# Performance work log

Hardware: AMD Instinct MI355X
Metric: run time of the kernel (lower is better)

Reference implementation:

```python
import jax, jax.numpy as jnp
import numpy as np

EPS = 1e-7
B, N, DIM, NH, HD, WIN, HASH_WIN = 2, 1024, 512, 8, 64, 64, 8


def expmap0(v, c):
    sqrt_c = jnp.clip(jnp.sqrt(c), EPS)
    v_norm = jnp.linalg.norm(v, axis=-1, keepdims=True)
    is_zero = v_norm < EPS
    safe = jnp.clip(v_norm, EPS)
    mag = jnp.tanh(sqrt_c * safe) / sqrt_c
    return jnp.where(is_zero, jnp.zeros_like(v), mag * (v / safe))


def poincare_dist(x, y, c):
    # x: (B,H,N,1,D), y: (B,H,N,W,D), c: (B,1,1,1,1) -> (B,H,N,W)
    sqrt_c = jnp.clip(jnp.sqrt(c), EPS)
    x2 = jnp.sum(x * x, -1, keepdims=True)
    y2 = jnp.sum(y * y, -1, keepdims=True)
    xy = jnp.sum(x * y, -1, keepdims=True)
    num = (1 - 2 * c * xy + c * y2) * x + (1 - c * x2) * (-y)
    den = 1 - 2 * c * xy + c * c * x2 * y2
    diff = num / jnp.clip(den, EPS)
    dn = jnp.linalg.norm(diff, axis=-1)
    arg = jnp.minimum(jnp.squeeze(sqrt_c, -1) * jnp.clip(dn, EPS), 1.0 - EPS)
    return 2.0 * jnp.arctanh(arg) / jnp.squeeze(sqrt_c, -1)


def sliding_windows(t, w):
    # t: (B,H,N,D) -> (B,H,N,w,D), left-padded causal window
    Bb, H, Nn, D = t.shape
    pad = jnp.zeros((Bb, H, w - 1, D), t.dtype)
    tp = jnp.concatenate([pad, t], axis=2)
    idx = jnp.arange(w)[None, :] + jnp.arange(Nn)[:, None]  # (N,w)
    return tp[:, :, idx, :]


def layernorm(x, s, b):
    m = jnp.mean(x, -1, keepdims=True)
    v = jnp.var(x, -1, keepdims=True)
    return (x - m) / jnp.sqrt(v + 1e-6) * s + b


def rope(x, cos, sin):
    # x: (B,N,H,hd), cos/sin: (N, hd//2) -- complex rotation in real arithmetic
    xr, xi = jnp.split(x, 2, axis=-1)
    cos = cos[None, :, None, :]
    sin = sin[None, :, None, :]
    return jnp.concatenate([xr * cos - xi * sin, xr * sin + xi * cos], axis=-1)


def setup_inputs() -> dict:
    key = jax.random.key(0)
    ks = jax.random.split(key, 10)
    x = jax.random.normal(ks[0], (B, N, DIM), jnp.float32)
    pos = jnp.arange(N, dtype=jnp.float32)
    inv = 1.0 / (10000.0 ** (jnp.arange(0, HD, 2, dtype=jnp.float32) / HD))
    ang = pos[:, None] * inv[None, :]  # (N, HD//2)
    freqs_cos, freqs_sin = jnp.cos(ang), jnp.sin(ang)
    c = jax.random.uniform(ks[1], (B,), jnp.float32) * 0.9 + 0.1
    s = 0.02
    Wq = jax.random.normal(ks[2], (DIM, DIM), jnp.float32) * s
    Wk = jax.random.normal(ks[3], (DIM, DIM), jnp.float32) * s
    Wv = jax.random.normal(ks[4], (DIM, DIM), jnp.float32) * s
    Wo = jax.random.normal(ks[5], (DIM, DIM), jnp.float32) * s
    W1 = jax.random.normal(ks[6], (DIM, 4 * DIM), jnp.float32) * s
    W2 = jax.random.normal(ks[7], (4 * DIM, DIM), jnp.float32) * s
    bq = jnp.zeros((DIM,)); bk = jnp.zeros((DIM,)); bv = jnp.zeros((DIM,))
    bo = jnp.zeros((DIM,)); b1 = jnp.zeros((4 * DIM,)); b2 = jnp.zeros((DIM,))
    ln1_s = jnp.ones((DIM,)); ln1_b = jnp.zeros((DIM,))
    ln2_s = jnp.ones((DIM,)); ln2_b = jnp.zeros((DIM,))
    geo_scale = jnp.ones((NH, 1, 1), jnp.float32)
    hash_offset = jax.random.normal(ks[8], (1, 1, NH, HD), jnp.float32) * 0.01
    return dict(x=x, freqs_cos=freqs_cos, freqs_sin=freqs_sin, c=c,
                Wq=Wq, bq=bq, Wk=Wk, bk=bk, Wv=Wv, bv=bv, Wo=Wo, bo=bo,
                W1=W1, b1=b1, W2=W2, b2=b2,
                ln1_s=ln1_s, ln1_b=ln1_b, ln2_s=ln2_s, ln2_b=ln2_b,
                geo_scale=geo_scale, hash_offset=hash_offset)


def reference(x, freqs_cos, freqs_sin, c, Wq, bq, Wk, bk, Wv, bv, Wo, bo,
              W1, b1, W2, b2, ln1_s, ln1_b, ln2_s, ln2_b, geo_scale, hash_offset):
    x_res = x
    xn = layernorm(x, ln1_s, ln1_b)
    q = (xn @ Wq + bq).reshape(B, N, NH, HD)
    k = (xn @ Wk + bk).reshape(B, N, NH, HD)
    v = (xn @ Wv + bv).reshape(B, N, NH, HD)
    q = q + hash_offset * jnp.log(1.0 + HASH_WIN)
    q_rot = rope(q, freqs_cos, freqs_sin)
    k_rot = rope(k, freqs_cos, freqs_sin)
    c_b = c.reshape(B, 1, 1, 1)
    q_h = expmap0(q_rot, c_b)
    k_h = expmap0(k_rot, c_b)
    q_h, k_h, v = (t.transpose(0, 2, 1, 3) for t in (q_h, k_h, v))  # (B,H,N,D)
    k_win = sliding_windows(k_h, WIN)  # (B,H,N,W,D)
    v_win = sliding_windows(v, WIN)
    dist = poincare_dist(q_h[:, :, :, None, :], k_win, c.reshape(B, 1, 1, 1, 1))  # (B,H,N,W)
    scores = -geo_scale * dist
    w = jax.nn.softmax(scores, axis=-1)
    attn = jnp.einsum('bhnw,bhnwd->bhnd', w, v_win)
    attn = attn.transpose(0, 2, 1, 3).reshape(B, N, DIM)
    x_out = x_res + (attn @ Wo + bo)
    h = layernorm(x_out, ln2_s, ln2_b)
    ffn = jax.nn.gelu(h @ W1 + b1) @ W2 + b2
    return x_out + ffn
```

## Files before the change

kernel.cpp:

```cpp
#include <hip/hip_runtime.h>
#include <math.h>
#include <stdint.h>

#define Bn   2
#define Nn   1024
#define DIMn 512
#define NHn  8
#define HDn  64
#define QKVS 1536
#define EPSF 1e-7f

typedef __attribute__((ext_vector_type(8))) short short8;
typedef __attribute__((ext_vector_type(4))) float floatx4;

__device__ __forceinline__ unsigned short f2bf(float f) {
  union { float f; uint32_t u; } v; v.f = f;
  uint32_t u = v.u;
  return (unsigned short)((u + 0x7FFFu + ((u >> 16) & 1u)) >> 16);
}
__device__ __forceinline__ float bf2f(unsigned short h) {
  union { uint32_t u; float f; } v; v.u = ((uint32_t)h) << 16;
  return v.f;
}

__device__ __forceinline__ float wsum(float v) {
#pragma unroll
  for (int m = 32; m >= 1; m >>= 1) v += __shfl_xor(v, m, 64);
  return v;
}
__device__ __forceinline__ float wmax(float v) {
#pragma unroll
  for (int m = 32; m >= 1; m >>= 1) v = fmaxf(v, __shfl_xor(v, m, 64));
  return v;
}

__device__ __forceinline__ float gelu_tanh(float x) {
  const float k0 = 0.7978845608028654f;
  float x3 = x * x * x;
  return 0.5f * x * (1.f + tanhf(k0 * (x + 0.044715f * x3)));
}

__device__ __forceinline__ void glds16(const unsigned short* g, unsigned short* l) {
  __builtin_amdgcn_global_load_lds((const __attribute__((address_space(1))) void*)g,
                                   (__attribute__((address_space(3))) void*)l, 16, 0, 0);
}

__global__ __launch_bounds__(256) void prep_kernel(
    const float* __restrict__ Wq, const float* __restrict__ Wk,
    const float* __restrict__ Wv, const float* __restrict__ Wo,
    const float* __restrict__ W1, const float* __restrict__ W2,
    unsigned short* __restrict__ Wcat_hi, unsigned short* __restrict__ Wcat_lo,
    unsigned short* __restrict__ Wo_t, unsigned short* __restrict__ W1_t,
    unsigned short* __restrict__ W2_t,
    const float* __restrict__ bq, const float* __restrict__ bk,
    const float* __restrict__ bv, float* __restrict__ bias_cat,
    const float* __restrict__ x, const float* __restrict__ ln1s,
    const float* __restrict__ ln1b,
    unsigned short* __restrict__ xn_hi, unsigned short* __restrict__ xn_lo) {
  __shared__ float t[32][33];
  __shared__ float red[2][4];
  int bid = blockIdx.x;
  int tid = threadIdx.x;
  if (bid == 3072) {
    for (int i = tid; i < 512; i += 256) {
      bias_cat[i] = bq[i];
      bias_cat[512 + i] = bk[i];
      bias_cat[1024 + i] = bv[i];
    }
    return;
  }
  if (bid > 3072) {
    int row = bid - 3073;
    const float* xr = x + (size_t)row * DIMn;
    float2 xv = *(const float2*)(xr + tid * 2);
    float s  = xv.x + xv.y;
    float s2 = xv.x * xv.x + xv.y * xv.y;
    s = wsum(s); s2 = wsum(s2);
    int wv = tid >> 6;
    if ((tid & 63) == 0) { red[0][wv] = s; red[1][wv] = s2; }
    __syncthreads();
    s  = red[0][0] + red[0][1] + red[0][2] + red[0][3];
    s2 = red[1][0] + red[1][1] + red[1][2] + red[1][3];
    float mean = s * (1.f / DIMn);
    float var  = s2 * (1.f / DIMn) - mean * mean;
    float rstd = rsqrtf(var + 1e-6f);
    int d = tid * 2;
    float2 gv = *(const float2*)(ln1s + d);
    float2 bv2 = *(const float2*)(ln1b + d);
    float o0 = (xv.x - mean) * rstd * gv.x + bv2.x;
    float o1 = (xv.y - mean) * rstd * gv.y + bv2.y;
    size_t idx = (size_t)row * DIMn + d;
    unsigned short h0 = f2bf(o0), h1 = f2bf(o1);
    ushort2 hv; hv.x = h0; hv.y = h1;
    *(ushort2*)(xn_hi + idx) = hv;
    ushort2 lv; lv.x = f2bf(o0 - bf2f(h0)); lv.y = f2bf(o1 - bf2f(h1));
    *(ushort2*)(xn_lo + idx) = lv;
    return;
  }
  const float* W;
  unsigned short* hi;
  unsigned short* lo = nullptr;
  int K, N, tix;
  if (bid < 256)       { W = Wq; hi = Wcat_hi;               lo = Wcat_lo;               K = 512;  N = 512;  tix = bid; }
  else if (bid < 512)  { W = Wk; hi = Wcat_hi + 512 * 512;   lo = Wcat_lo + 512 * 512;   K = 512;  N = 512;  tix = bid - 256; }
  else if (bid < 768)  { W = Wv; hi = Wcat_hi + 1024 * 512;  K = 512;  N = 512;  tix = bid - 512; }
  else if (bid < 1024) { W = Wo; hi = Wo_t;                  K = 512;  N = 512;  tix = bid - 768; }
  else if (bid < 2048) { W = W1; hi = W1_t;                  K = 512;  N = 2048; tix = bid - 1024; }
  else                 { W = W2; hi = W2_t;                  K = 2048; N = 512;  tix = bid - 2048; }
  int ntn = N >> 5;
  int kt = tix / ntn, nt = tix - kt * ntn;
  int k0 = kt * 32, n0 = nt * 32;
  for (int i = tid; i < 1024; i += 256) {
    int r = i >> 5, c = i & 31;
    t[r][c] = W[(size_t)(k0 + r) * N + n0 + c];
  }
  __syncthreads();
  for (int i = tid; i < 1024; i += 256) {
    int r = i >> 5, c = i & 31;
    float v = t[c][r];
    unsigned short h = f2bf(v);
    size_t oi = (size_t)(n0 + r) * K + k0 + c;
    hi[oi] = h;
    if (lo) lo[oi] = f2bf(v - bf2f(h));
  }
}

__global__ __launch_bounds__(256) void ln_kernel(const float* __restrict__ x,
                                                 const float* __restrict__ g,
                                                 const float* __restrict__ be,
                                                 unsigned short* __restrict__ yhi) {
  __shared__ float red[2][4];
  int row = blockIdx.x;
  int tid = threadIdx.x;
  const float* xr = x + (size_t)row * DIMn;
  float2 xv = *(const float2*)(xr + tid * 2);
  float s  = xv.x + xv.y;
  float s2 = xv.x * xv.x + xv.y * xv.y;
  s = wsum(s); s2 = wsum(s2);
  int wv = tid >> 6;
  if ((tid & 63) == 0) { red[0][wv] = s; red[1][wv] = s2; }
  __syncthreads();
  s  = red[0][0] + red[0][1] + red[0][2] + red[0][3];
  s2 = red[1][0] + red[1][1] + red[1][2] + red[1][3];
  float mean = s * (1.f / DIMn);
  float var  = s2 * (1.f / DIMn) - mean * mean;
  float rstd = rsqrtf(var + 1e-6f);
  int d = tid * 2;
  float2 gv = *(const float2*)(g + d);
  float2 bv = *(const float2*)(be + d);
  float o0 = (xv.x - mean) * rstd * gv.x + bv.x;
  float o1 = (xv.y - mean) * rstd * gv.y + bv.y;
  size_t idx = (size_t)row * DIMn + d;
  ushort2 hv; hv.x = f2bf(o0); hv.y = f2bf(o1);
  *(ushort2*)(yhi + idx) = hv;
}

template <int BM, int BN, int BKT, int SPLIT, int EPI, int OUTBF16>
__global__ __launch_bounds__(256) void gemm_mfma(
    const unsigned short* __restrict__ Ahi, const unsigned short* __restrict__ Alo,
    const unsigned short* __restrict__ Bhi, const unsigned short* __restrict__ Blo,
    const float* __restrict__ bias, const float* __restrict__ res,
    void* __restrict__ outp, int M, int N, int K) {
  constexpr int FI = BM / 32, FJ = BN / 32;
  constexpr int AE = BM * BKT, BE = BN * BKT;
  constexpr int NB = (SPLIT > 0) ? 2 : 1;
  constexpr int CPR = BKT / 8;
  constexpr int ACH = BM * CPR, BCH = BN * CPR;
  __shared__ unsigned short smem[NB * (AE + BE)];
  unsigned short* AsHi = smem;
  unsigned short* AsLo = smem + ((SPLIT > 0) ? AE : 0);
  unsigned short* BsHi = smem + NB * AE;
  unsigned short* BsLo = BsHi + ((SPLIT > 0) ? BE : 0);

  int tid = threadIdx.x;
  int lane = tid & 63;
  int wid = tid >> 6;
  int wm = (wid >> 1) * (BM / 2), wn = (wid & 1) * (BN / 2);
  int bm = blockIdx.y * BM, bn = blockIdx.x * BN;
  int m16 = lane & 15, kg = lane >> 4;
  bool dos = (SPLIT == 1) || (SPLIT == 2 && bn < 1024);

  floatx4 acc[FI][FJ];
#pragma unroll
  for (int i = 0; i < FI; ++i)
#pragma unroll
    for (int j = 0; j < FJ; ++j) { floatx4 z = {0.f, 0.f, 0.f, 0.f}; acc[i][j] = z; }

  const unsigned short* aph = Ahi + (size_t)bm * K;
  const unsigned short* bph = Bhi + (size_t)bn * K;
  const unsigned short* apl = (SPLIT > 0) ? (Alo + (size_t)bm * K) : nullptr;
  const unsigned short* bpl = (SPLIT > 0) ? (Blo + (size_t)bn * K) : nullptr;

  for (int k0 = 0; k0 < K; k0 += BKT) {
#pragma unroll
    for (int c = tid; c < ACH; c += 256) {
      int row = c / CPR, kk = (c % CPR) * 8;
      glds16(aph + (size_t)row * K + k0 + kk, AsHi + c * 8);
      if (SPLIT > 0 && dos) glds16(apl + (size_t)row * K + k0 + kk, AsLo + c * 8);
    }
#pragma unroll
    for (int c = tid; c < BCH; c += 256) {
      int row = c / CPR, kk = (c % CPR) * 8;
      glds16(bph + (size_t)row * K + k0 + kk, BsHi + c * 8);
      if (SPLIT > 0 && dos) glds16(bpl + (size_t)row * K + k0 + kk, BsLo + c * 8);
    }
    __syncthreads();

#pragma unroll
    for (int ks = 0; ks < BKT / 32; ++ks) {
      short8 ah[FI], bh[FJ];
      short8 al[(SPLIT > 0) ? FI : 1], bl[(SPLIT > 0) ? FJ : 1];
#pragma unroll
      for (int i = 0; i < FI; ++i) {
        int r = wm + i * 16 + m16;
        ah[i] = *(const short8*)&AsHi[r * BKT + ks * 32 + kg * 8];
        if (SPLIT > 0 && dos) al[i] = *(const short8*)&AsLo[r * BKT + ks * 32 + kg * 8];
      }
#pragma unroll
      for (int j = 0; j < FJ; ++j) {
        int r = wn + j * 16 + m16;
        bh[j] = *(const short8*)&BsHi[r * BKT + ks * 32 + kg * 8];
        if (SPLIT > 0 && dos) bl[j] = *(const short8*)&BsLo[r * BKT + ks * 32 + kg * 8];
      }
#pragma unroll
      for (int i = 0; i < FI; ++i)
#pragma unroll
        for (int j = 0; j < FJ; ++j) {
          acc[i][j] = __builtin_amdgcn_mfma_f32_16x16x32_bf16(ah[i], bh[j], acc[i][j], 0, 0, 0);
          if (SPLIT > 0) {
            if (dos) {
              acc[i][j] = __builtin_amdgcn_mfma_f32_16x16x32_bf16(al[i], bh[j], acc[i][j], 0, 0, 0);
              acc[i][j] = __builtin_amdgcn_mfma_f32_16x16x32_bf16(ah[i], bl[j], acc[i][j], 0, 0, 0);
            }
          }
        }
    }
    __syncthreads();
  }

#pragma unroll
  for (int i = 0; i < FI; ++i) {
    int gr0 = bm + wm + i * 16 + kg * 4;
#pragma unroll
    for (int j = 0; j < FJ; ++j) {
      int gc = bn + wn + j * 16 + m16;
      float bsv = bias[gc];
#pragma unroll
      for (int r = 0; r < 4; ++r) {
        size_t idx = (size_t)(gr0 + r) * N + gc;
        float v = acc[i][j][r] + bsv;
        if constexpr (EPI == 1) v += res[idx];
        if constexpr (EPI == 2) v = gelu_tanh(v);
        if constexpr (OUTBF16) ((unsigned short*)outp)[idx] = f2bf(v);
        else ((float*)outp)[idx] = v;
      }
    }
  }
}

__global__ __launch_bounds__(512) void attn_fused(const float* __restrict__ qkv,
                                                  const float* __restrict__ fcos,
                                                  const float* __restrict__ fsin,
                                                  const float* __restrict__ cvec,
                                                  const float* __restrict__ geo,
                                                  const float* __restrict__ hash,
                                                  unsigned short* __restrict__ attn_out) {
  __shared__ unsigned short Qhi[32][72], Qlo[32][72];
  __shared__ unsigned short Khi[96][72], Klo[96][72];
  __shared__ unsigned short Vt[64][104];
  __shared__ unsigned short Pb[32][104];
  __shared__ float Sf[32][97];
  __shared__ float x2s[32], bxs[32], y2s[96], gys[96];

  int tid = threadIdx.x, lane = tid & 63, wv = tid >> 6;
  int bid = blockIdx.x;
  int nt = bid & 31, h = (bid >> 5) & 7, b = bid >> 8;
  int n0 = nt * 32;
  float c = cvec[b];
  float sqc = sqrtf(c);
  float rsqc = 1.f / sqc;
  float gs = geo[h];
  int dr = lane & 31;
  bool hih = lane >= 32;
  const float LOG9 = 2.1972245773362196f;
  float hofr = hash[h * HDn + dr] * LOG9;
  float hofi = hash[h * HDn + dr + 32] * LOG9;

  for (int i = tid; i < 32 * 52; i += 512) ((uint32_t*)Pb)[i] = 0u;

#pragma unroll
  for (int i = 0; i < 4; ++i) {
    int q = wv * 4 + i;
    int n = n0 + q;
    size_t bas = (size_t)(b * Nn + n) * QKVS + h * HDn;
    float qr = qkv[bas + dr] + hofr;
    float qi = qkv[bas + dr + 32] + hofi;
    float cs = fcos[n * 32 + dr], sn = fsin[n * 32 + dr];
    float qv = hih ? (qr * sn + qi * cs) : (qr * cs - qi * sn);
    float nq = sqrtf(wsum(qv * qv));
    float sq = fmaxf(nq, EPSF);
    float t = sqc * sq;
    float em = expf(-2.f * t);
    float opem = 1.f + em;
    float mag = ((1.f - em) / opem) * rsqc;
    float sech2 = 4.f * em / (opem * opem);
    float oq = (nq < EPSF) ? 0.f : mag * (qv / sq);
    unsigned short hh = f2bf(oq);
    Qhi[q][lane] = hh;
    Qlo[q][lane] = f2bf(oq - bf2f(hh));
    if (lane == 0) {
      x2s[q] = (nq < EPSF) ? 0.f : mag * mag;
      bxs[q] = (nq < EPSF) ? 1.f : sech2;
    }
  }
#pragma unroll 4
  for (int i = 0; i < 12; ++i) {
    int r = wv * 12 + i;
    int gi = n0 - 64 + r;
    float ok = 0.f, vf = 0.f, y2 = 0.f, gy = 1.f;
    if (gi >= 0) {
      size_t bas = (size_t)(b * Nn + gi) * QKVS + h * HDn;
      float kr = qkv[bas + 512 + dr];
      float ki = qkv[bas + 512 + dr + 32];
      vf = qkv[bas + 1024 + lane];
      float cs = fcos[gi * 32 + dr], sn = fsin[gi * 32 + dr];
      float kv = hih ? (kr * sn + ki * cs) : (kr * cs - ki * sn);
      float nk = sqrtf(wsum(kv * kv));
      float sk = fmaxf(nk, EPSF);
      float t = sqc * sk;
      float em = expf(-2.f * t);
      float opem = 1.f + em;
      float mag = ((1.f - em) / opem) * rsqc;
      float sech2 = 4.f * em / (opem * opem);
      ok = (nk < EPSF) ? 0.f : mag * (kv / sk);
      y2 = (nk < EPSF) ? 0.f : mag * mag;
      gy = (nk < EPSF) ? 1.f : sech2;
    }
    unsigned short hh = f2bf(ok);
    Khi[r][lane] = hh;
    Klo[r][lane] = f2bf(ok - bf2f(hh));
    Vt[lane][r] = f2bf(vf);
    if (lane == 0) { y2s[r] = y2; gys[r] = gy; }
  }
  __syncthreads();

  int m16 = lane & 15, kg = lane >> 4;
#pragma unroll
  for (int uu = 0; uu < 2; ++uu) {
    int u = wv + uu * 8;
    if (u < 12) {
      int mt = u / 6, ntile = u % 6;
      floatx4 acc = {0.f, 0.f, 0.f, 0.f};
#pragma unroll
      for (int ks = 0; ks < 2; ++ks) {
        short8 ah = *(const short8*)&Qhi[mt * 16 + m16][ks * 32 + kg * 8];
        short8 al = *(const short8*)&Qlo[mt * 16 + m16][ks * 32 + kg * 8];
        short8 bh = *(const short8*)&Khi[ntile * 16 + m16][ks * 32 + kg * 8];
        short8 bl = *(const short8*)&Klo[ntile * 16 + m16][ks * 32 + kg * 8];
        acc = __builtin_amdgcn_mfma_f32_16x16x32_bf16(ah, bh, acc, 0, 0, 0);
        acc = __builtin_amdgcn_mfma_f32_16x16x32_bf16(al, bh, acc, 0, 0, 0);
        acc = __builtin_amdgcn_mfma_f32_16x16x32_bf16(ah, bl, acc, 0, 0, 0);
      }
#pragma unroll
      for (int r = 0; r < 4; ++r) Sf[mt * 16 + kg * 4 + r][ntile * 16 + m16] = acc[r];
    }
  }
  __syncthreads();

#pragma unroll
  for (int i = 0; i < 4; ++i) {
    int nl = wv * 4 + i;
    int r = nl + 1 + lane;
    float xy = Sf[nl][r];
    float x2 = x2s[nl], y2 = y2s[r];
    float bx = bxs[nl], gy = gys[r];

    float den = fmaf(c * c * x2, y2, fmaf(-2.f * c, xy, 1.f));
    den = fmaxf(den, EPSF);
    float rden = 1.f / den;
    float s2 = fmaxf(x2 - 2.f * xy + y2, 0.f);
    float z = sqrtf(c * s2 * rden);
    float omz2 = bx * gy * rden;
    float opz = 1.f + fminf(z, 1.f);
    float ratio = fminf(opz * opz / omz2, 1.9999999e7f);
    float sc = -gs * logf(ratio) * rsqc;

    float mx = wmax(sc);
    float e = expf(sc - mx);
    float se = wsum(e);
    Pb[nl][r] = f2bf(e / se);
  }
  __syncthreads();

  {
    int mt = wv >> 2, ntile = wv & 3;
    floatx4 acc = {0.f, 0.f, 0.f, 0.f};
#pragma unroll
    for (int ks = 0; ks < 3; ++ks) {
      short8 a = *(const short8*)&Pb[mt * 16 + m16][ks * 32 + kg * 8];
      short8 bb = *(const short8*)&Vt[ntile * 16 + m16][ks * 32 + kg * 8];
      acc = __builtin_amdgcn_mfma_f32_16x16x32_bf16(a, bb, acc, 0, 0, 0);
    }
#pragma unroll
    for (int r = 0; r < 4; ++r) {
      int qrow = mt * 16 + kg * 4 + r;
      int d = ntile * 16 + m16;
      attn_out[(size_t)(b * Nn + n0 + qrow) * DIMn + h * HDn + d] = f2bf(acc[r]);
    }
  }
}

extern "C" void kernel_launch(void* const* d_in, const int* in_sizes, int n_in,
                              void* d_out, int out_size, void* d_ws, size_t ws_size,
                              hipStream_t stream) {
  const float* x    = (const float*)d_in[0];
  const float* fcos = (const float*)d_in[1];
  const float* fsin = (const float*)d_in[2];
  const float* cvec = (const float*)d_in[3];
  const float* Wq = (const float*)d_in[4];  const float* bq = (const float*)d_in[5];
  const float* Wk = (const float*)d_in[6];  const float* bk = (const float*)d_in[7];
  const float* Wv = (const float*)d_in[8];  const float* bv = (const float*)d_in[9];
  const float* Wo = (const float*)d_in[10]; const float* bo = (const float*)d_in[11];
  const float* W1 = (const float*)d_in[12]; const float* b1 = (const float*)d_in[13];
  const float* W2 = (const float*)d_in[14]; const float* b2 = (const float*)d_in[15];
  const float* ln1s = (const float*)d_in[16]; const float* ln1b = (const float*)d_in[17];
  const float* ln2s = (const float*)d_in[18]; const float* ln2b = (const float*)d_in[19];
  const float* geo  = (const float*)d_in[20]; const float* hash = (const float*)d_in[21];
  float* out = (float*)d_out;
  char* base = (char*)d_ws;

  unsigned short* Wcat_hi = (unsigned short*)(base + 0);
  unsigned short* Wcat_lo = (unsigned short*)(base + 1572864);
  unsigned short* Wo_t    = (unsigned short*)(base + 3145728);
  unsigned short* W1_t    = (unsigned short*)(base + 3670016);
  unsigned short* W2_t    = (unsigned short*)(base + 5767168);
  unsigned short* xn_hi   = (unsigned short*)(base + 7864320);
  unsigned short* xn_lo   = (unsigned short*)(base + 9961472);
  float*          qkv     = (float*)(base + 12058624);
  unsigned short* attnb   = (unsigned short*)(base + 7864320);
  float*          xout    = (float*)(base + 9961472);
  unsigned short* hbuf    = (unsigned short*)(base + 14155776);
  unsigned short* mid     = (unsigned short*)(base + 16252928);
  float*          bias_cat= (float*)(base + 24641536);

  const int M = Bn * Nn;

  prep_kernel<<<3073 + M, 256, 0, stream>>>(Wq, Wk, Wv, Wo, W1, W2, Wcat_hi, Wcat_lo,
                                            Wo_t, W1_t, W2_t, bq, bk, bv, bias_cat,
                                            x, ln1s, ln1b, xn_hi, xn_lo);
  gemm_mfma<64, 64, 32, 2, 0, 0><<<dim3(QKVS / 64, M / 64), 256, 0, stream>>>(
      xn_hi, xn_lo, Wcat_hi, Wcat_lo, bias_cat, nullptr, qkv, M, QKVS, 512);
  attn_fused<<<Bn * NHn * (Nn / 32), 512, 0, stream>>>(qkv, fcos, fsin, cvec, geo, hash, attnb);
  gemm_mfma<32, 64, 64, 0, 1, 0><<<dim3(DIMn / 64, M / 32), 256, 0, stream>>>(
      attnb, nullptr, Wo_t, nullptr, bo, x, xout, M, DIMn, 512);
  ln_kernel<<<M, 256, 0, stream>>>(xout, ln2s, ln2b, hbuf);
  gemm_mfma<64, 128, 64, 0, 2, 1><<<dim3(2048 / 128, M / 64), 256, 0, stream>>>(
      hbuf, nullptr, W1_t, nullptr, b1, nullptr, mid, M, 2048, 512);
  gemm_mfma<32, 64, 64, 0, 1, 0><<<dim3(DIMn / 64, M / 32), 256, 0, stream>>>(
      mid, nullptr, W2_t, nullptr, b2, xout, out, M, DIMn, 2048);
}
```

Measured before the change: 194.2 us.

## Fuse LayerNorm2 into FFN1 GEMM prologue and deepen K tiles for output GEMMs

Removes the standalone ln_kernel and its bf16 hbuf round trip. A new ffn1_ln kernel computes per-row mean and rstd for its 64-row tile, then normalizes fp32 xout on the fly while filling shared memory before the MFMA loop. Each of the 16 column blocks now recomputes the row statistics and rereads fp32 activations instead of bf16, which trades extra global reads for one fewer launch and one fewer intermediate write. Separately, the Wo and W2 GEMMs use a K tile of 128 instead of 64.

Result: slower. 215.4 us (+11.0%).

```diff
diff --git a/kernel.cpp b/kernel.cpp
--- a/kernel.cpp
+++ b/kernel.cpp
@@ -125,36 +125,6 @@
   }
 }
 
-__global__ __launch_bounds__(256) void ln_kernel(const float* __restrict__ x,
-                                                 const float* __restrict__ g,
-                                                 const float* __restrict__ be,
-                                                 unsigned short* __restrict__ yhi) {
-  __shared__ float red[2][4];
-  int row = blockIdx.x;
-  int tid = threadIdx.x;
-  const float* xr = x + (size_t)row * DIMn;
-  float2 xv = *(const float2*)(xr + tid * 2);
-  float s  = xv.x + xv.y;
-  float s2 = xv.x * xv.x + xv.y * xv.y;
-  s = wsum(s); s2 = wsum(s2);
-  int wv = tid >> 6;
-  if ((tid & 63) == 0) { red[0][wv] = s; red[1][wv] = s2; }
-  __syncthreads();
-  s  = red[0][0] + red[0][1] + red[0][2] + red[0][3];
-  s2 = red[1][0] + red[1][1] + red[1][2] + red[1][3];
-  float mean = s * (1.f / DIMn);
-  float var  = s2 * (1.f / DIMn) - mean * mean;
-  float rstd = rsqrtf(var + 1e-6f);
-  int d = tid * 2;
-  float2 gv = *(const float2*)(g + d);
-  float2 bv = *(const float2*)(be + d);
-  float o0 = (xv.x - mean) * rstd * gv.x + bv.x;
-  float o1 = (xv.y - mean) * rstd * gv.y + bv.y;
-  size_t idx = (size_t)row * DIMn + d;
-  ushort2 hv; hv.x = f2bf(o0); hv.y = f2bf(o1);
-  *(ushort2*)(yhi + idx) = hv;
-}
-
 template <int BM, int BN, int BKT, int SPLIT, int EPI, int OUTBF16>
 __global__ __launch_bounds__(256) void gemm_mfma(
     const unsigned short* __restrict__ Ahi, const unsigned short* __restrict__ Alo,
@@ -253,6 +223,113 @@
         if constexpr (EPI == 2) v = gelu_tanh(v);
         if constexpr (OUTBF16) ((unsigned short*)outp)[idx] = f2bf(v);
         else ((float*)outp)[idx] = v;
+      }
+    }
+  }
+}
+
+__global__ __launch_bounds__(256) void ffn1_ln(
+    const float* __restrict__ xout, const float* __restrict__ g,
+    const float* __restrict__ be,
+    const unsigned short* __restrict__ W1t, const float* __restrict__ b1,
+    unsigned short* __restrict__ mid) {
+  constexpr int BM = 64, BN = 128, BK = 64;
+  constexpr int AST = BK + 8;
+  __shared__ unsigned short As[BM * AST];
+  __shared__ unsigned short Bs[BN * BK];
+  __shared__ float mrs[BM][2];
+
+  int tid = threadIdx.x, lane = tid & 63, wid = tid >> 6;
+  int bm = blockIdx.y * BM, bn = blockIdx.x * BN;
+  int m16 = lane & 15, kg = lane >> 4;
+  int wm = (wid >> 1) * (BM / 2), wn = (wid & 1) * (BN / 2);
+
+#pragma unroll 4
+  for (int i = 0; i < 16; ++i) {
+    int row = wid * 16 + i;
+    const float* xr = xout + (size_t)(bm + row) * DIMn;
+    float4 a = ((const float4*)xr)[lane * 2];
+    float4 b = ((const float4*)xr)[lane * 2 + 1];
+    float s  = a.x + a.y + a.z + a.w + b.x + b.y + b.z + b.w;
+    float s2 = a.x*a.x + a.y*a.y + a.z*a.z + a.w*a.w + b.x*b.x + b.y*b.y + b.z*b.z + b.w*b.w;
+    s = wsum(s); s2 = wsum(s2);
+    if (lane == 0) {
+      float mean = s * (1.f / DIMn);
+      float var  = s2 * (1.f / DIMn) - mean * mean;
+      mrs[row][0] = mean;
+      mrs[row][1] = rsqrtf(var + 1e-6f);
+    }
+  }
+  __syncthreads();
+
+  floatx4 acc[2][4];
+#pragma unroll
+  for (int i = 0; i < 2; ++i)
+#pragma unroll
+    for (int j = 0; j < 4; ++j) { floatx4 z = {0.f, 0.f, 0.f, 0.f}; acc[i][j] = z; }
+
+  for (int k0 = 0; k0 < DIMn; k0 += BK) {
+    {
+      int row = tid >> 2, c0 = (tid & 3) * 16;
+      const float* xr = xout + (size_t)(bm + row) * DIMn + k0 + c0;
+      float mean = mrs[row][0], rstd = mrs[row][1];
+      unsigned short* dst = &As[row * AST + c0];
+#pragma unroll
+      for (int j = 0; j < 2; ++j) {
+        float4 v0 = ((const float4*)xr)[j * 2];
+        float4 v1 = ((const float4*)xr)[j * 2 + 1];
+        float4 g0 = ((const float4*)(g + k0 + c0))[j * 2];
+        float4 g1 = ((const float4*)(g + k0 + c0))[j * 2 + 1];
+        float4 e0 = ((const float4*)(be + k0 + c0))[j * 2];
+        float4 e1 = ((const float4*)(be + k0 + c0))[j * 2 + 1];
+        short8 o;
+        o[0] = (short)f2bf((v0.x - mean) * rstd * g0.x + e0.x);
+        o[1] = (short)f2bf((v0.y - mean) * rstd * g0.y + e0.y);
+        o[2] = (short)f2bf((v0.z - mean) * rstd * g0.z + e0.z);
+        o[3] = (short)f2bf((v0.w - mean) * rstd * g0.w + e0.w);
+        o[4] = (short)f2bf((v1.x - mean) * rstd * g1.x + e1.x);
+        o[5] = (short)f2bf((v1.y - mean) * rstd * g1.y + e1.y);
+        o[6] = (short)f2bf((v1.z - mean) * rstd * g1.z + e1.z);
+        o[7] = (short)f2bf((v1.w - mean) * rstd * g1.w + e1.w);
+        *(short8*)(dst + j * 8) = o;
+      }
+    }
+#pragma unroll
+    for (int c = tid; c < BN * 8; c += 256) {
+      int row = c >> 3, kk = (c & 7) * 8;
+      glds16(W1t + (size_t)(bn + row) * DIMn + k0 + kk, Bs + c * 8);
+    }
+    __syncthreads();
+
+#pragma unroll
+    for (int ks = 0; ks < 2; ++ks) {
+      short8 ah[2], bh[4];
+#pragma unroll
+      for (int i = 0; i < 2; ++i)
+        ah[i] = *(const short8*)&As[(wm + i * 16 + m16) * AST + ks * 32 + kg * 8];
+#pragma unroll
+      for (int j = 0; j < 4; ++j)
+        bh[j] = *(const short8*)&Bs[(wn + j * 16 + m16) * BK + ks * 32 + kg * 8];
+#pragma unroll
+      for (int i = 0; i < 2; ++i)
+#pragma unroll
+        for (int j = 0; j < 4; ++j)
+          acc[i][j] = __builtin_amdgcn_mfma_f32_16x16x32_bf16(ah[i], bh[j], acc[i][j], 0, 0, 0);
+    }
+    __syncthreads();
+  }
+
+#pragma unroll
+  for (int i = 0; i < 2; ++i) {
+    int gr0 = bm + wm + i * 16 + kg * 4;
+#pragma unroll
+    for (int j = 0; j < 4; ++j) {
+      int gc = bn + wn + j * 16 + m16;
+      float bsv = b1[gc];
+#pragma unroll
+      for (int r = 0; r < 4; ++r) {
+        float v = gelu_tanh(acc[i][j][r] + bsv);
+        mid[(size_t)(gr0 + r) * 2048 + gc] = f2bf(v);
       }
     }
   }
@@ -439,7 +516,6 @@
   float*          qkv     = (float*)(base + 12058624);
   unsigned short* attnb   = (unsigned short*)(base + 7864320);
   float*          xout    = (float*)(base + 9961472);
-  unsigned short* hbuf    = (unsigned short*)(base + 14155776);
   unsigned short* mid     = (unsigned short*)(base + 16252928);
   float*          bias_cat= (float*)(base + 24641536);
 
@@ -451,11 +527,10 @@
   gemm_mfma<64, 64, 32, 2, 0, 0><<<dim3(QKVS / 64, M / 64), 256, 0, stream>>>(
       xn_hi, xn_lo, Wcat_hi, Wcat_lo, bias_cat, nullptr, qkv, M, QKVS, 512);
   attn_fused<<<Bn * NHn * (Nn / 32), 512, 0, stream>>>(qkv, fcos, fsin, cvec, geo, hash, attnb);
-  gemm_mfma<32, 64, 64, 0, 1, 0><<<dim3(DIMn / 64, M / 32), 256, 0, stream>>>(
+  gemm_mfma<32, 64, 128, 0, 1, 0><<<dim3(DIMn / 64, M / 32), 256, 0, stream>>>(
       attnb, nullptr, Wo_t, nullptr, bo, x, xout, M, DIMn, 512);
-  ln_kernel<<<M, 256, 0, stream>>>(xout, ln2s, ln2b, hbuf);
-  gemm_mfma<64, 128, 64, 0, 2, 1><<<dim3(2048 / 128, M / 64), 256, 0, stream>>>(
-      hbuf, nullptr, W1_t, nullptr, b1, nullptr, mid, M, 2048, 512);
-  gemm_mfma<32, 64, 64, 0, 1, 0><<<dim3(DIMn / 64, M / 32), 256, 0, stream>>>(
+  ffn1_ln<<<dim3(2048 / 128, M / 64), 256, 0, stream>>>(
+      xout, ln2s, ln2b, W1_t, b1, mid);
+  gemm_mfma<32, 64, 128, 0, 1, 0><<<dim3(DIMn / 64, M / 32), 256, 0, stream>>>(
       mid, nullptr, W2_t, nullptr, b2, xout, out, M, DIMn, 2048);
 }
```

## Fuse all stages into one persistent cooperative megakernel with grid syncs

Applied to the files above, without the earlier changes.

Replaces the seven separate kernel launches (prep, QKV GEMM, attention, out-proj, layernorm, FFN GEMMs) with a single cooperative kernel that loops over work units per stage and uses grid.sync between stages. The intent is to remove launch overhead and inter-kernel gaps for this small, latency-bound problem. It trades that for grid-wide barrier cost, 512-thread blocks reusing one shared-memory union, and a grid capped at 512 blocks, which can leave stages with fewer tiles than their previous launches. The old multi-kernel path is kept as a fallback if the cooperative launch fails.

New measurement: 477.4 us. +145.9%, slower.

```diff
diff --git a/kernel.cpp b/kernel.cpp
--- a/kernel.cpp
+++ b/kernel.cpp
@@ -1,4 +1,5 @@
 #include <hip/hip_runtime.h>
+#include <hip/hip_cooperative_groups.h>
 #include <math.h>
 #include <stdint.h>
 
@@ -13,6 +14,8 @@
 typedef __attribute__((ext_vector_type(8))) short short8;
 typedef __attribute__((ext_vector_type(4))) float floatx4;
 
+namespace cg = cooperative_groups;
+
 __device__ __forceinline__ unsigned short f2bf(float f) {
   union { float f; uint32_t u; } v; v.f = f;
   uint32_t u = v.u;
@@ -43,6 +46,378 @@
 __device__ __forceinline__ void glds16(const unsigned short* g, unsigned short* l) {
   __builtin_amdgcn_global_load_lds((const __attribute__((address_space(1))) void*)g,
                                    (__attribute__((address_space(3))) void*)l, 16, 0, 0);
+}
+
+struct MegaArgs {
+  const float *x, *fcos, *fsin, *cvec;
+  const float *Wq, *bq, *Wk, *bk, *Wv, *bv, *Wo, *bo, *W1, *b1, *W2, *b2;
+  const float *ln1s, *ln1b, *ln2s, *ln2b, *geo, *hash;
+  float* out;
+  unsigned short *Wcat_hi, *Wcat_lo, *Wo_t, *W1_t, *W2_t;
+  unsigned short *xn_hi, *xn_lo, *attnb, *hbuf, *mid;
+  float *qkv, *xout, *bias_cat;
+};
+
+struct AttnSm {
+  unsigned short Qhi[32][72], Qlo[32][72];
+  unsigned short Khi[96][72], Klo[96][72];
+  unsigned short Vt[64][104];
+  unsigned short Pb[32][104];
+  float Sf[32][97];
+  float x2s[32], bxs[32], y2s[96], gys[96];
+};
+struct PrepSm { float t[32][33]; float red[2][8]; };
+union MegaSm {
+  PrepSm prep;
+  AttnSm attn;
+  unsigned short gbuf[12288];
+};
+
+template <int BM, int BN, int BKT, int SPLIT, int EPI, int OUTBF16>
+__device__ void gemm_tile(unsigned short* sbuf, int bm, int bn,
+    const unsigned short* __restrict__ Ahi, const unsigned short* __restrict__ Alo,
+    const unsigned short* __restrict__ Bhi, const unsigned short* __restrict__ Blo,
+    const float* __restrict__ bias, const float* __restrict__ res,
+    void* __restrict__ outp, int N, int K, int tid) {
+  constexpr int FI = BM / 32, FJ = BN / 64;
+  constexpr int AE = BM * BKT, BE = BN * BKT;
+  constexpr int NB = (SPLIT > 0) ? 2 : 1;
+  constexpr int CPR = BKT / 8;
+  constexpr int ACH = BM * CPR, BCH = BN * CPR;
+  unsigned short* AsHi = sbuf;
+  unsigned short* AsLo = sbuf + ((SPLIT > 0) ? AE : 0);
+  unsigned short* BsHi = sbuf + NB * AE;
+  unsigned short* BsLo = BsHi + ((SPLIT > 0) ? BE : 0);
+
+  int lane = tid & 63, wid = tid >> 6;
+  int wm = (wid >> 2) * (BM / 2), wn = (wid & 3) * (BN / 4);
+  int m16 = lane & 15, kg = lane >> 4;
+  bool dos = (SPLIT == 1) || (SPLIT == 2 && bn < 1024);
+
+  floatx4 acc[FI][FJ];
+#pragma unroll
+  for (int i = 0; i < FI; ++i)
+#pragma unroll
+    for (int j = 0; j < FJ; ++j) { floatx4 z = {0.f, 0.f, 0.f, 0.f}; acc[i][j] = z; }
+
+  const unsigned short* aph = Ahi + (size_t)bm * K;
+  const unsigned short* bph = Bhi + (size_t)bn * K;
+  const unsigned short* apl = (SPLIT > 0) ? (Alo + (size_t)bm * K) : nullptr;
+  const unsigned short* bpl = (SPLIT > 0) ? (Blo + (size_t)bn * K) : nullptr;
+
+  for (int k0 = 0; k0 < K; k0 += BKT) {
+    for (int c = tid; c < ACH; c += 512) {
+      int row = c / CPR, kk = (c % CPR) * 8;
+      glds16(aph + (size_t)row * K + k0 + kk, AsHi + c * 8);
+      if (SPLIT > 0 && dos) glds16(apl + (size_t)row * K + k0 + kk, AsLo + c * 8);
+    }
+    for (int c = tid; c < BCH; c += 512) {
+      int row = c / CPR, kk = (c % CPR) * 8;
+      glds16(bph + (size_t)row * K + k0 + kk, BsHi + c * 8);
+      if (SPLIT > 0 && dos) glds16(bpl + (size_t)row * K + k0 + kk, BsLo + c * 8);
+    }
+    __syncthreads();
+
+#pragma unroll
+    for (int ks = 0; ks < BKT / 32; ++ks) {
+      short8 ah[FI], bh[FJ];
+      short8 al[(SPLIT > 0) ? FI : 1], bl[(SPLIT > 0) ? FJ : 1];
+#pragma unroll
+      for (int i = 0; i < FI; ++i) {
+        int r = wm + i * 16 + m16;
+        ah[i] = *(const short8*)&AsHi[r * BKT + ks * 32 + kg * 8];
+        if (SPLIT > 0 && dos) al[i] = *(const short8*)&AsLo[r * BKT + ks * 32 + kg * 8];
+      }
+#pragma unroll
+      for (int j = 0; j < FJ; ++j) {
+        int r = wn + j * 16 + m16;
+        bh[j] = *(const short8*)&BsHi[r * BKT + ks * 32 + kg * 8];
+        if (SPLIT > 0 && dos) bl[j] = *(const short8*)&BsLo[r * BKT + ks * 32 + kg * 8];
+      }
+#pragma unroll
+      for (int i = 0; i < FI; ++i)
+#pragma unroll
+        for (int j = 0; j < FJ; ++j) {
+          acc[i][j] = __builtin_amdgcn_mfma_f32_16x16x32_bf16(ah[i], bh[j], acc[i][j], 0, 0, 0);
+          if (SPLIT > 0 && dos) {
+            acc[i][j] = __builtin_amdgcn_mfma_f32_16x16x32_bf16(al[i], bh[j], acc[i][j], 0, 0, 0);
+            acc[i][j] = __builtin_amdgcn_mfma_f32_16x16x32_bf16(ah[i], bl[j], acc[i][j], 0, 0, 0);
+          }
+        }
+    }
+    __syncthreads();
+  }
+
+#pragma unroll
+  for (int i = 0; i < FI; ++i) {
+    int gr0 = bm + wm + i * 16 + kg * 4;
+#pragma unroll
+    for (int j = 0; j < FJ; ++j) {
+      int gc = bn + wn + j * 16 + m16;
+      float bsv = bias[gc];
+#pragma unroll
+      for (int r = 0; r < 4; ++r) {
+        size_t idx = (size_t)(gr0 + r) * N + gc;
+        float v = acc[i][j][r] + bsv;
+        if constexpr (EPI == 1) v += res[idx];
+        if constexpr (EPI == 2) v = gelu_tanh(v);
+        if constexpr (OUTBF16) ((unsigned short*)outp)[idx] = f2bf(v);
+        else ((float*)outp)[idx] = v;
+      }
+    }
+  }
+}
+
+__global__ __launch_bounds__(512, 4) void mega(MegaArgs A) {
+  cg::grid_group grid = cg::this_grid();
+  __shared__ MegaSm sm;
+  int tid = threadIdx.x;
+  int lane = tid & 63, wid = tid >> 6;
+  int nblk = gridDim.x;
+
+  for (int u = blockIdx.x; u < 3073 + 2048; u += nblk) {
+    if (u == 3072) {
+      if (tid < 512) {
+        A.bias_cat[tid] = A.bq[tid];
+        A.bias_cat[512 + tid] = A.bk[tid];
+        A.bias_cat[1024 + tid] = A.bv[tid];
+      }
+    } else if (u > 3072) {
+      int row = u - 3073;
+      const float* xr = A.x + (size_t)row * DIMn;
+      float xv = xr[tid];
+      float s = wsum(xv), s2 = wsum(xv * xv);
+      if (lane == 0) { sm.prep.red[0][wid] = s; sm.prep.red[1][wid] = s2; }
+      __syncthreads();
+      s = 0.f; s2 = 0.f;
+#pragma unroll
+      for (int w = 0; w < 8; ++w) { s += sm.prep.red[0][w]; s2 += sm.prep.red[1][w]; }
+      float mean = s * (1.f / DIMn);
+      float var  = s2 * (1.f / DIMn) - mean * mean;
+      float rstd = rsqrtf(var + 1e-6f);
+      float o = (xv - mean) * rstd * A.ln1s[tid] + A.ln1b[tid];
+      size_t idx = (size_t)row * DIMn + tid;
+      unsigned short h = f2bf(o);
+      A.xn_hi[idx] = h;
+      A.xn_lo[idx] = f2bf(o - bf2f(h));
+      __syncthreads();
+    } else {
+      const float* W;
+      unsigned short* hi;
+      unsigned short* lo = nullptr;
+      int K, N, tix;
+      if (u < 256)       { W = A.Wq; hi = A.Wcat_hi;              lo = A.Wcat_lo;              K = 512;  N = 512;  tix = u; }
+      else if (u < 512)  { W = A.Wk; hi = A.Wcat_hi + 512 * 512;  lo = A.Wcat_lo + 512 * 512;  K = 512;  N = 512;  tix = u - 256; }
+      else if (u < 768)  { W = A.Wv; hi = A.Wcat_hi + 1024 * 512; K = 512;  N = 512;  tix = u - 512; }
+      else if (u < 1024) { W = A.Wo; hi = A.Wo_t;                 K = 512;  N = 512;  tix = u - 768; }
+      else if (u < 2048) { W = A.W1; hi = A.W1_t;                 K = 512;  N = 2048; tix = u - 1024; }
+      else               { W = A.W2; hi = A.W2_t;                 K = 2048; N = 512;  tix = u - 2048; }
+      int ntn = N >> 5;
+      int kt = tix / ntn, nt = tix - kt * ntn;
+      int k0 = kt * 32, n0 = nt * 32;
+      for (int i = tid; i < 1024; i += 512) {
+        int r = i >> 5, c = i & 31;
+        sm.prep.t[r][c] = W[(size_t)(k0 + r) * N + n0 + c];
+      }
+      __syncthreads();
+      for (int i = tid; i < 1024; i += 512) {
+        int r = i >> 5, c = i & 31;
+        float v = sm.prep.t[c][r];
+        unsigned short h = f2bf(v);
+        size_t oi = (size_t)(n0 + r) * K + k0 + c;
+        hi[oi] = h;
+        if (lo) lo[oi] = f2bf(v - bf2f(h));
+      }
+      __syncthreads();
+    }
+  }
+  grid.sync();
+
+  for (int u = blockIdx.x; u < 768; u += nblk) {
+    int ty = u / 24, tx = u - ty * 24;
+    gemm_tile<64, 64, 32, 2, 0, 0>(sm.gbuf, ty * 64, tx * 64,
+        A.xn_hi, A.xn_lo, A.Wcat_hi, A.Wcat_lo, A.bias_cat, nullptr,
+        A.qkv, QKVS, 512, tid);
+  }
+  grid.sync();
+
+  for (int u = blockIdx.x; u < 512; u += nblk) {
+    AttnSm& at = sm.attn;
+    int nt = u & 31, h = (u >> 5) & 7, b = u >> 8;
+    int n0 = nt * 32;
+    float c = A.cvec[b];
+    float sqc = sqrtf(c);
+    float rsqc = 1.f / sqc;
+    float gs = A.geo[h];
+    int dr = lane & 31;
+    bool hih = lane >= 32;
+    const float LOG9 = 2.1972245773362196f;
+    float hofr = A.hash[h * HDn + dr] * LOG9;
+    float hofi = A.hash[h * HDn + dr + 32] * LOG9;
+
+    for (int i = tid; i < 32 * 52; i += 512) ((uint32_t*)at.Pb)[i] = 0u;
+
+#pragma unroll
+    for (int i = 0; i < 4; ++i) {
+      int q = wid * 4 + i;
+      int n = n0 + q;
+      size_t bas = (size_t)(b * Nn + n) * QKVS + h * HDn;
+      float qr = A.qkv[bas + dr] + hofr;
+      float qi = A.qkv[bas + dr + 32] + hofi;
+      float cs = A.fcos[n * 32 + dr], sn = A.fsin[n * 32 + dr];
+      float qv = hih ? (qr * sn + qi * cs) : (qr * cs - qi * sn);
+      float nq = sqrtf(wsum(qv * qv));
+      float sq = fmaxf(nq, EPSF);
+      float t = sqc * sq;
+      float em = expf(-2.f * t);
+      float opem = 1.f + em;
+      float mag = ((1.f - em) / opem) * rsqc;
+      float sech2 = 4.f * em / (opem * opem);
+      float oq = (nq < EPSF) ? 0.f : mag * (qv / sq);
+      unsigned short hh = f2bf(oq);
+      at.Qhi[q][lane] = hh;
+      at.Qlo[q][lane] = f2bf(oq - bf2f(hh));
+      if (lane == 0) {
+        at.x2s[q] = (nq < EPSF) ? 0.f : mag * mag;
+        at.bxs[q] = (nq < EPSF) ? 1.f : sech2;
+      }
+    }
+#pragma unroll 4
+    for (int i = 0; i < 12; ++i) {
+      int r = wid * 12 + i;
+      int gi = n0 - 64 + r;
+      float ok = 0.f, vf = 0.f, y2 = 0.f, gy = 1.f;
+      if (gi >= 0) {
+        size_t bas = (size_t)(b * Nn + gi) * QKVS + h * HDn;
+        float kr = A.qkv[bas + 512 + dr];
+        float ki = A.qkv[bas + 512 + dr + 32];
+        vf = A.qkv[bas + 1024 + lane];
+        float cs = A.fcos[gi * 32 + dr], sn = A.fsin[gi * 32 + dr];
+        float kv = hih ? (kr * sn + ki * cs) : (kr * cs - ki * sn);
+        float nk = sqrtf(wsum(kv * kv));
+        float sk = fmaxf(nk, EPSF);
+        float t = sqc * sk;
+        float em = expf(-2.f * t);
+        float opem = 1.f + em;
+        float mag = ((1.f - em) / opem) * rsqc;
+        float sech2 = 4.f * em / (opem * opem);
+        ok = (nk < EPSF) ? 0.f : mag * (kv / sk);
+        y2 = (nk < EPSF) ? 0.f : mag * mag;
+        gy = (nk < EPSF) ? 1.f : sech2;
+      }
+      unsigned short hh = f2bf(ok);
+      at.Khi[r][lane] = hh;
+      at.Klo[r][lane] = f2bf(ok - bf2f(hh));
+      at.Vt[lane][r] = f2bf(vf);
+      if (lane == 0) { at.y2s[r] = y2; at.gys[r] = gy; }
+    }
+    __syncthreads();
+
+    int m16 = lane & 15, kg = lane >> 4;
+#pragma unroll
+    for (int uu = 0; uu < 2; ++uu) {
+      int tu = wid + uu * 8;
+      if (tu < 12) {
+        int mt = tu / 6, ntile = tu % 6;
+        floatx4 acc = {0.f, 0.f, 0.f, 0.f};
+#pragma unroll
+        for (int ks = 0; ks < 2; ++ks) {
+          short8 ah = *(const short8*)&at.Qhi[mt * 16 + m16][ks * 32 + kg * 8];
+          short8 al = *(const short8*)&at.Qlo[mt * 16 + m16][ks * 32 + kg * 8];
+          short8 bh = *(const short8*)&at.Khi[ntile * 16 + m16][ks * 32 + kg * 8];
+          short8 bl = *(const short8*)&at.Klo[ntile * 16 + m16][ks * 32 + kg * 8];
+          acc = __builtin_amdgcn_mfma_f32_16x16x32_bf16(ah, bh, acc, 0, 0, 0);
+          acc = __builtin_amdgcn_mfma_f32_16x16x32_bf16(al, bh, acc, 0, 0, 0);
+          acc = __builtin_amdgcn_mfma_f32_16x16x32_bf16(ah, bl, acc, 0, 0, 0);
+        }
+#pragma unroll
+        for (int r = 0; r < 4; ++r) at.Sf[mt * 16 + kg * 4 + r][ntile * 16 + m16] = acc[r];
+      }
+    }
+    __syncthreads();
+
+#pragma unroll
+    for (int i = 0; i < 4; ++i) {
+      int nl = wid * 4 + i;
+      int r = nl + 1 + lane;
+      float xy = at.Sf[nl][r];
+      float x2 = at.x2s[nl], y2 = at.y2s[r];
+      float bx = at.bxs[nl], gy = at.gys[r];
+
+      float den = fmaf(c * c * x2, y2, fmaf(-2.f * c, xy, 1.f));
+      den = fmaxf(den, EPSF);
+      float rden = 1.f / den;
+      float s2 = fmaxf(x2 - 2.f * xy + y2, 0.f);
+      float z = sqrtf(c * s2 * rden);
+      float omz2 = bx * gy * rden;
+      float opz = 1.f + fminf(z, 1.f);
+      float ratio = fminf(opz * opz / omz2, 1.9999999e7f);
+      float sc = -gs * logf(ratio) * rsqc;
+
+      float mx = wmax(sc);
+      float e = expf(sc - mx);
+      float se = wsum(e);
+      at.Pb[nl][r] = f2bf(e / se);
+    }
+    __syncthreads();
+
+    {
+      int mt = wid >> 2, ntile = wid & 3;
+      floatx4 acc = {0.f, 0.f, 0.f, 0.f};
+#pragma unroll
+      for (int ks = 0; ks < 3; ++ks) {
+        short8 a = *(const short8*)&at.Pb[mt * 16 + m16][ks * 32 + kg * 8];
+        short8 bb = *(const short8*)&at.Vt[ntile * 16 + m16][ks * 32 + kg * 8];
+        acc = __builtin_amdgcn_mfma_f32_16x16x32_bf16(a, bb, acc, 0, 0, 0);
+      }
+#pragma unroll
+      for (int r = 0; r < 4; ++r) {
+        int qrow = mt * 16 + kg * 4 + r;
+        int d = ntile * 16 + m16;
+        A.attnb[(size_t)(b * Nn + n0 + qrow) * DIMn + h * HDn + d] = f2bf(acc[r]);
+      }
+    }
+    __syncthreads();
+  }
+  grid.sync();
+
+  for (int u = blockIdx.x; u < 512; u += nblk) {
+    int ty = u >> 3, tx = u & 7;
+    gemm_tile<32, 64, 64, 0, 1, 0>(sm.gbuf, ty * 32, tx * 64,
+        A.attnb, nullptr, A.Wo_t, nullptr, A.bo, A.x, A.xout, DIMn, 512, tid);
+  }
+  grid.sync();
+
+  for (int u = blockIdx.x; u < 2048; u += nblk) {
+    const float* xr = A.xout + (size_t)u * DIMn;
+    float xv = xr[tid];
+    float s = wsum(xv), s2 = wsum(xv * xv);
+    if (lane == 0) { sm.prep.red[0][wid] = s; sm.prep.red[1][wid] = s2; }
+    __syncthreads();
+    s = 0.f; s2 = 0.f;
+#pragma unroll
+    for (int w = 0; w < 8; ++w) { s += sm.prep.red[0][w]; s2 += sm.prep.red[1][w]; }
+    float mean = s * (1.f / DIMn);
+    float var  = s2 * (1.f / DIMn) - mean * mean;
+    float rstd = rsqrtf(var + 1e-6f);
+    float o = (xv - mean) * rstd * A.ln2s[tid] + A.ln2b[tid];
+    A.hbuf[(size_t)u * DIMn + tid] = f2bf(o);
+    __syncthreads();
+  }
+  grid.sync();
+
+  for (int u = blockIdx.x; u < 512; u += nblk) {
+    int ty = u >> 4, tx = u & 15;
+    gemm_tile<64, 128, 64, 0, 2, 1>(sm.gbuf, ty * 64, tx * 128,
+        A.hbuf, nullptr, A.W1_t, nullptr, A.b1, nullptr, A.mid, 2048, 512, tid);
+  }
+  grid.sync();
+
+  for (int u = blockIdx.x; u < 512; u += nblk) {
+    int ty = u >> 3, tx = u & 7;
+    gemm_tile<32, 64, 64, 0, 1, 0>(sm.gbuf, ty * 32, tx * 64,
+        A.mid, nullptr, A.W2_t, nullptr, A.b2, A.xout, A.out, DIMn, 2048, tid);
+  }
 }
 
 __global__ __launch_bounds__(256) void prep_kernel(
@@ -227,11 +602,9 @@
 #pragma unroll
         for (int j = 0; j < FJ; ++j) {
           acc[i][j] = __builtin_amdgcn_mfma_f32_16x16x32_bf16(ah[i], bh[j], acc[i][j], 0, 0, 0);
-          if (SPLIT > 0) {
-            if (dos) {
-              acc[i][j] = __builtin_amdgcn_mfma_f32_16x16x32_bf16(al[i], bh[j], acc[i][j], 0, 0, 0);
-              acc[i][j] = __builtin_amdgcn_mfma_f32_16x16x32_bf16(ah[i], bl[j], acc[i][j], 0, 0, 0);
-            }
+          if (SPLIT > 0 && dos) {
+            acc[i][j] = __builtin_amdgcn_mfma_f32_16x16x32_bf16(al[i], bh[j], acc[i][j], 0, 0, 0);
+            acc[i][j] = __builtin_amdgcn_mfma_f32_16x16x32_bf16(ah[i], bl[j], acc[i][j], 0, 0, 0);
           }
         }
     }
@@ -445,6 +818,28 @@
 
   const int M = Bn * Nn;
 
+  MegaArgs A;
+  A.x = x; A.fcos = fcos; A.fsin = fsin; A.cvec = cvec;
+  A.Wq = Wq; A.bq = bq; A.Wk = Wk; A.bk = bk; A.Wv = Wv; A.bv = bv;
+  A.Wo = Wo; A.bo = bo; A.W1 = W1; A.b1 = b1; A.W2 = W2; A.b2 = b2;
+  A.ln1s = ln1s; A.ln1b = ln1b; A.ln2s = ln2s; A.ln2b = ln2b;
+  A.geo = geo; A.hash = hash; A.out = out;
+  A.Wcat_hi = Wcat_hi; A.Wcat_lo = Wcat_lo; A.Wo_t = Wo_t; A.W1_t = W1_t; A.W2_t = W2_t;
+  A.xn_hi = xn_hi; A.xn_lo = xn_lo; A.attnb = attnb; A.hbuf = hbuf; A.mid = mid;
+  A.qkv = qkv; A.xout = xout; A.bias_cat = bias_cat;
+
+  int occ = 0;
+  hipError_t qe = hipOccupancyMaxActiveBlocksPerMultiprocessor(
+      &occ, reinterpret_cast<const void*>(mega), 512, 0);
+  if (qe != hipSuccess || occ < 1) occ = 1;
+  int grid = occ * 256;
+  if (grid > 512) grid = 512;
+
+  void* kargs[1] = { (void*)&A };
+  hipError_t le = hipLaunchCooperativeKernel(
+      reinterpret_cast<const void*>(mega), dim3(grid), dim3(512), kargs, 0, stream);
+  if (le == hipSuccess) return;
+
   prep_kernel<<<3073 + M, 256, 0, stream>>>(Wq, Wk, Wv, Wo, W1, W2, Wcat_hi, Wcat_lo,
                                             Wo_t, W1_t, W2_t, bq, bk, bv, bias_cat,
                                             x, ln1s, ln1b, xn_hi, xn_lo);
```
